# Kernel optimization log

Hardware: AMD Instinct MI355X
Metric: run time of the kernel (lower is better)

Reference implementation:

```python
import jax, jax.numpy as jnp
import numpy as np
from jax import lax

DIM = 192
NUM_CLASSES = 4
D_INNER = 2 * DIM          # expand=2
D_STATE = 16
D_CONV = 4
DT_RANK = (DIM + 15) // 16  # ceil(192/16)=12
PATCH = 16


def _mamba_params(key, prefix):
    ks = jax.random.split(key, 9)
    s = lambda k, shape, scale: (jax.random.normal(k, shape, jnp.float32) * scale)
    p = {
        prefix + '_in_w':   s(ks[0], (2 * D_INNER, DIM), 0.02),
        prefix + '_conv_w': s(ks[1], (D_INNER, D_CONV), 0.1),
        prefix + '_conv_b': jnp.zeros((D_INNER,), jnp.float32),
        prefix + '_xproj_w': s(ks[2], (DT_RANK + 2 * D_STATE, D_INNER), 0.02),
        prefix + '_dt_w':   s(ks[3], (D_INNER, DT_RANK), 0.1),
        prefix + '_dt_b':   s(ks[4], (D_INNER,), 0.1),
        # A_log init: log(1..d_state) broadcast over d_inner (mamba default)
        prefix + '_A_log':  jnp.broadcast_to(jnp.log(jnp.arange(1, D_STATE + 1, dtype=jnp.float32)), (D_INNER, D_STATE)) + 0.0,
        prefix + '_D':      jnp.ones((D_INNER,), jnp.float32),
        prefix + '_out_w':  s(ks[5], (DIM, D_INNER), 0.02),
    }
    return p


def setup_inputs() -> dict:
    key = jax.random.key(0)
    ks = jax.random.split(key, 8)
    inp = {
        'x': jax.random.normal(ks[0], (32, 3, 384, 384), jnp.float32),
        'patch_w': jax.random.normal(ks[1], (DIM, 3, PATCH, PATCH), jnp.float32) * 0.02,
        'patch_b': jnp.zeros((DIM,), jnp.float32),
        'ln_g': jnp.ones((DIM,), jnp.float32),
        'ln_b': jnp.zeros((DIM,), jnp.float32),
        'fc_w': jax.random.normal(ks[2], (NUM_CLASSES, DIM), jnp.float32) * 0.02,
        'fc_b': jnp.zeros((NUM_CLASSES,), jnp.float32),
    }
    inp.update(_mamba_params(ks[3], 'f'))
    inp.update(_mamba_params(ks[4], 'b'))
    return inp


def _layernorm(x, g, b, eps=1e-5):
    mu = jnp.mean(x, -1, keepdims=True)
    var = jnp.mean(jnp.square(x - mu), -1, keepdims=True)
    return (x - mu) * lax.rsqrt(var + eps) * g + b


def _mamba(x, in_w, conv_w, conv_b, xproj_w, dt_w, dt_b, A_log, Dskip, out_w):
    # x: [B, L, DIM]
    Bn, L, _ = x.shape
    xz = x @ in_w.T                                    # [B, L, 2*di]
    xi, z = jnp.split(xz, 2, axis=-1)
    # causal depthwise conv1d, kernel D_CONV, left pad
    xp = jnp.pad(xi, ((0, 0), (D_CONV - 1, 0), (0, 0)))
    xc = conv_b + sum(xp[:, k:k + L, :] * conv_w[:, k] for k in range(D_CONV))
    xc = jax.nn.silu(xc)                               # [B, L, di]
    proj = xc @ xproj_w.T                              # [B, L, dtr+2*ds]
    dt, Bm, Cm = jnp.split(proj, [DT_RANK, DT_RANK + D_STATE], axis=-1)
    dt = jax.nn.softplus(dt @ dt_w.T + dt_b)           # [B, L, di]
    A = -jnp.exp(A_log)                                # [di, ds]

    def step(h, inp):
        dt_t, B_t, C_t, x_t = inp                      # [B,di],[B,ds],[B,ds],[B,di]
        dA = jnp.exp(dt_t[:, :, None] * A)             # [B, di, ds]
        h = dA * h + (dt_t * x_t)[:, :, None] * B_t[:, None, :]
        y = jnp.einsum('bds,bs->bd', h, C_t)
        return h, y

    h0 = jnp.zeros((Bn, D_INNER, D_STATE), x.dtype)
    xs = (dt.transpose(1, 0, 2), Bm.transpose(1, 0, 2),
          Cm.transpose(1, 0, 2), xc.transpose(1, 0, 2))
    _, ys = lax.scan(step, h0, xs)                     # [L, B, di]
    y = ys.transpose(1, 0, 2) + xc * Dskip
    y = y * jax.nn.silu(z)
    return y @ out_w.T                                 # [B, L, DIM]


def reference(x, patch_w, patch_b, ln_g, ln_b, fc_w, fc_b,
              f_in_w, f_conv_w, f_conv_b, f_xproj_w, f_dt_w, f_dt_b, f_A_log, f_D, f_out_w,
              b_in_w, b_conv_w, b_conv_b, b_xproj_w, b_dt_w, b_dt_b, b_A_log, b_D, b_out_w):
    Bn, C, H, W = x.shape
    Hp, Wp = H // PATCH, W // PATCH
    # patch embed: stride==kernel conv == reshape + einsum
    xr = x.reshape(Bn, C, Hp, PATCH, Wp, PATCH)
    tok = jnp.einsum('bchpwq,dcpq->bhwd', xr, patch_w) + patch_b
    tok = tok.reshape(Bn, Hp * Wp, DIM)                # [B, L, D]
    tok = _layernorm(tok, ln_g, ln_b)
    fwd = _mamba(tok, f_in_w, f_conv_w, f_conv_b, f_xproj_w, f_dt_w, f_dt_b, f_A_log, f_D, f_out_w)
    bwd = _mamba(tok[:, ::-1, :], b_in_w, b_conv_w, b_conv_b, b_xproj_w, b_dt_w, b_dt_b, b_A_log, b_D, b_out_w)
    out = fwd + bwd[:, ::-1, :]
    pooled = jnp.mean(out, axis=1)                     # adaptive avg pool to 1
    return pooled @ fc_w.T + fc_b                      # [B, num_classes]
```

## Files before the change

kernel.cpp:

```cpp
#include <hip/hip_runtime.h>
#include <hip/hip_bf16.h>

#define NC 32
#define CL 18

typedef __attribute__((ext_vector_type(8))) short short8;
typedef __attribute__((ext_vector_type(4))) float f32x4;
typedef __attribute__((ext_vector_type(2))) float f32x2;

__device__ __forceinline__ float sigm(float x){ return 1.0f/(1.0f+__expf(-x)); }

__device__ __forceinline__ ushort f2bf(float f){
  unsigned u = __float_as_uint(f);
  unsigned r = (u + 0x7fffu + ((u>>16)&1u)) >> 16;
  return (ushort)r;
}
__device__ __forceinline__ float bf2f(ushort h){ return __uint_as_float(((unsigned)h)<<16); }

__global__ __launch_bounds__(256) void k_prep_all(
    const float* __restrict__ patch_w, const float* __restrict__ f_in_w,
    const float* __restrict__ b_in_w,
    const float* __restrict__ f_xw, const float* __restrict__ b_xw,
    const float* __restrict__ f_cw, const float* __restrict__ b_cw,
    const float* __restrict__ f_al, const float* __restrict__ b_al,
    const float* __restrict__ fc_w, const float* __restrict__ f_ow,
    const float* __restrict__ b_ow,
    ushort* __restrict__ pw_h, ushort* __restrict__ pw_l,
    ushort* __restrict__ iw_h, ushort* __restrict__ iw_l,
    ushort* __restrict__ xw_h, ushort* __restrict__ xw_l,
    float* __restrict__ cwT, float* __restrict__ Abuf,
    float* __restrict__ A0fl, float* __restrict__ W2){
  const int bx = blockIdx.x, t = threadIdx.x;
  if (bx < 1728){
    int which = bx/576;
    int i = (bx - which*576)*256 + t;
    if (which==0){
      float f = patch_w[i];
      ushort hb = f2bf(f);
      pw_h[i]=hb; pw_l[i]=f2bf(f - bf2f(hb));
    } else {
      const float* src = (which==1) ? f_in_w : b_in_w;
      int dirofs = (which==1) ? 0 : 48;
      float f = src[i];
      int n = i/192, k = i%192;
      int nblk = n>>4, r = n&15, kblk = k>>5, kk = k&31;
      int lane = r + ((kk>>3)<<4), j = kk&7;
      size_t idx = ((size_t)((nblk+dirofs)*6 + kblk)*64 + lane)*8 + j;
      ushort hb = f2bf(f);
      iw_h[idx]=hb; iw_l[idx]=f2bf(f - bf2f(hb));
    }
  } else if (bx < 1872){
    int i = (bx-1728)*256 + t;
    int dir=i/(48*384), rem=i%(48*384), n=rem/384, k=rem%384;
    float v = (n<44) ? (dir?b_xw:f_xw)[n*384+k] : 0.f;
    ushort hb = f2bf(v);
    xw_h[i]=hb; xw_l[i]=f2bf(v - bf2f(hb));
  } else if (bx < 1884){
    int i = (bx-1872)*256 + t;
    int dir=i/1536, rem=i%1536, j=rem/384, k=rem%384;
    cwT[i] = (dir ? b_cw : f_cw)[k*4+j];
  } else if (bx < 1887){
    int i = (bx-1884)*256 + t;
    if (i < 768){
      int dir=i/384, di=i%384;
      const float* alp = (dir?b_al:f_al) + di*16;
      float A0 = -expf(alp[0]);
      bool fast = true;
      Abuf[(size_t)i*16] = A0;
      #pragma unroll
      for (int s=1;s<16;s++){
        float A = -expf(alp[s]);
        Abuf[(size_t)i*16+s] = A;
        fast = fast && (fabsf(A - (s+1)*A0) <= 1e-5f*(s+1)*fabsf(A0));
      }
      A0fl[i*2]=A0; A0fl[i*2+1]=fast?1.f:0.f;
    }
  } else {
    int i = (bx-1887)*256 + t;
    if (i < 768){
      int dir=i/384, di=i%384;
      const float* ow = dir ? b_ow : f_ow;
      float a0=0.f,a1=0.f,a2=0.f,a3=0.f;
      for (int d=0; d<192; ++d){
        float o = ow[d*384 + di];
        a0 += fc_w[0*192+d]*o; a1 += fc_w[1*192+d]*o;
        a2 += fc_w[2*192+d]*o; a3 += fc_w[3*192+d]*o;
      }
      W2[(0*2+dir)*384+di]=a0; W2[(1*2+dir)*384+di]=a1;
      W2[(2*2+dir)*384+di]=a2; W2[(3*2+dir)*384+di]=a3;
    }
  }
}
__device__ __forceinline__ float w2at(const float* W2, int dir, int ch, int di){
  return W2[(ch*2+dir)*384+di];
}

__global__ __launch_bounds__(1024) void k_patch(
    const float* __restrict__ x,
    const ushort* __restrict__ pw_h, const ushort* __restrict__ pw_l,
    const float* __restrict__ pb, const float* __restrict__ lng,
    const float* __restrict__ lnb,
    ushort* __restrict__ tokf_h, ushort* __restrict__ tokf_l,
    int b0, int Mc){
  __shared__ __align__(16) char sBmem[49152];
  __shared__ __align__(16) ushort sAh[64*64], sAl[64*64];
  __shared__ float sLN[4][64][2];
  ushort* sBh = (ushort*)sBmem;
  ushort* sBl = (ushort*)(sBmem + 24576);
  const int tid = threadIdx.x;
  const int m0 = blockIdx.x*64;
  const int lane = tid&63, w = tid>>6;
  const int wr = w>>2, wc = w&3;
  const int r = lane&15, g = lane>>4;
  f32x4 acc[3];
  #pragma unroll
  for (int i=0;i<3;i++) acc[i] = (f32x4){0.f,0.f,0.f,0.f};

  for (int s=0;s<12;s++){
    const int c = s>>2, p0 = (s&3)*4;
    {
      int f = tid;
      int m = f>>4, rem = f&15, pp = rem>>2, qq = rem&3;
      int rm = m0 + m;
      float4 v = make_float4(0.f,0.f,0.f,0.f);
      if (rm < Mc){
        int b = b0 + rm/576, l = rm%576, hp = l/24, wp = l%24;
        size_t idx4 = ((size_t)((b*3+c)*384) + hp*16 + p0+pp)*96 + wp*4 + qq;
        v = reinterpret_cast<const float4*>(x)[idx4];
      }
      ushort4 hv, lv;
      hv.x=f2bf(v.x); lv.x=f2bf(v.x-bf2f(hv.x));
      hv.y=f2bf(v.y); lv.y=f2bf(v.y-bf2f(hv.y));
      hv.z=f2bf(v.z); lv.z=f2bf(v.z-bf2f(hv.z));
      hv.w=f2bf(v.w); lv.w=f2bf(v.w-bf2f(hv.w));
      int byte = (m*128 + pp*32 + qq*8) ^ ((m&7)<<4);
      *reinterpret_cast<ushort4*>((char*)sAh + byte) = hv;
      *reinterpret_cast<ushort4*>((char*)sAl + byte) = lv;
    }
    #pragma unroll
    for (int i=0;i<2;i++){
      int f = tid + i*1024;
      if (f < 1536){
        int n = f>>3, k8 = f&7;
        size_t gi = (size_t)n*768 + s*64 + k8*8;
        uint4 bh = *reinterpret_cast<const uint4*>(pw_h + gi);
        uint4 bl = *reinterpret_cast<const uint4*>(pw_l + gi);
        int byte = (n*128 + k8*16) ^ ((n&7)<<4);
        *reinterpret_cast<uint4*>((char*)sBh + byte) = bh;
        *reinterpret_cast<uint4*>((char*)sBl + byte) = bl;
      }
    }
    __syncthreads();
    #pragma unroll
    for (int kk=0;kk<2;kk++){
      int arow = wr*16 + r;
      int abyte = (arow*128 + kk*64 + g*16) ^ ((arow&7)<<4);
      short8 ah = *reinterpret_cast<const short8*>((char*)sAh + abyte);
      short8 al = *reinterpret_cast<const short8*>((char*)sAl + abyte);
      #pragma unroll
      for (int nfl=0; nfl<3; nfl++){
        int brow = (wc*3+nfl)*16 + r;
        int bbyte = (brow*128 + kk*64 + g*16) ^ ((brow&7)<<4);
        short8 bh = *reinterpret_cast<const short8*>((char*)sBh + bbyte);
        short8 bll = *reinterpret_cast<const short8*>((char*)sBl + bbyte);
        acc[nfl] = __builtin_amdgcn_mfma_f32_16x16x32_bf16(ah, bh, acc[nfl], 0,0,0);
        acc[nfl] = __builtin_amdgcn_mfma_f32_16x16x32_bf16(ah, bll, acc[nfl], 0,0,0);
        acc[nfl] = __builtin_amdgcn_mfma_f32_16x16x32_bf16(al, bh, acc[nfl], 0,0,0);
      }
    }
    __syncthreads();
  }
  float pbv[3], gv[3], bv[3];
  #pragma unroll
  for (int nfl=0;nfl<3;nfl++){
    int col = (wc*3+nfl)*16 + r;
    pbv[nfl]=pb[col]; gv[nfl]=lng[col]; bv[nfl]=lnb[col];
  }
  #pragma unroll
  for (int nfl=0;nfl<3;nfl++)
    #pragma unroll
    for (int q=0;q<4;q++) acc[nfl][q] += pbv[nfl];
  float sum[4]={0,0,0,0}, sq[4]={0,0,0,0};
  #pragma unroll
  for (int nfl=0;nfl<3;nfl++)
    #pragma unroll
    for (int q=0;q<4;q++){ float v=acc[nfl][q]; sum[q]+=v; sq[q]+=v*v; }
  #pragma unroll
  for (int off=1; off<16; off<<=1){
    #pragma unroll
    for (int q=0;q<4;q++){
      sum[q]+=__shfl_xor(sum[q],off);
      sq[q] +=__shfl_xor(sq[q],off);
    }
  }
  if (r==0){
    #pragma unroll
    for (int q=0;q<4;q++){
      int row = wr*16 + g*4 + q;
      sLN[wc][row][0]=sum[q]; sLN[wc][row][1]=sq[q];
    }
  }
  __syncthreads();
  float* sT = (float*)sBmem;
  #pragma unroll
  for (int q=0;q<4;q++){
    int rl = wr*16 + g*4 + q;
    float stot = sLN[0][rl][0]+sLN[1][rl][0]+sLN[2][rl][0]+sLN[3][rl][0];
    float qtot = sLN[0][rl][1]+sLN[1][rl][1]+sLN[2][rl][1]+sLN[3][rl][1];
    float mu = stot*(1.f/192.f);
    float var = qtot*(1.f/192.f) - mu*mu;
    float rs = rsqrtf(var + 1e-5f);
    #pragma unroll
    for (int nfl=0;nfl<3;nfl++)
      sT[rl*192 + (wc*3+nfl)*16 + r] = (acc[nfl][q]-mu)*rs*gv[nfl] + bv[nfl];
  }
  __syncthreads();
  const int mB = m0>>4;
  #pragma unroll
  for (int i=0;i<2;i++){
    int fl = tid + 1024*i;
    if (fl < 1536){
      int mb = fl/384, rem = fl-mb*384, kb = rem>>6, ln = rem&63;
      int rr = ln&15, gq = ln>>4;
      const float* sp = sT + (mb*16+rr)*192 + kb*32 + gq*8;
      short8 hv, lv;
      #pragma unroll
      for (int j=0;j<8;j++){
        float v = sp[j];
        ushort hb = f2bf(v);
        hv[j] = (short)hb;
        lv[j] = (short)f2bf(v - bf2f(hb));
      }
      size_t o = ((size_t)((mB+mb)*6 + kb)*64 + ln)*8;
      *reinterpret_cast<short8*>(tokf_h + o) = hv;
      *reinterpret_cast<short8*>(tokf_l + o) = lv;
// ... 144 lines not shown
  for (int kc=0; kc<6; ++kc){
    #pragma unroll
    for (int i=0;i<5;i++){
      int f = tid + i*256;
      if (f < 67*16){
        int rr = f>>4, kq = f&15;
        int l = l0 + rr - 3;
        float4 v = make_float4(0.f,0.f,0.f,0.f);
        if (l >= 0) v = *reinterpret_cast<const float4*>(xib + (seq+l)*384 + kc*64 + kq*4);
        int kqs = kq ^ (rr&15);
        *reinterpret_cast<float4*>(sRaw + rr*64 + kqs*4) = v;
      }
    }
    __syncthreads();
    #pragma unroll
    for (int i=0;i<4;i++){
      int f = tid + i*256;
      int m = f>>4, kq = f&15;
      float4 a = reinterpret_cast<const float4*>(cbp)[kc*16 + kq];
      #pragma unroll
      for (int j=0;j<4;j++){
        int rr = m + j;
        float4 rv = *reinterpret_cast<const float4*>(sRaw + rr*64 + (kq ^ (rr&15))*4);
        float4 cv = reinterpret_cast<const float4*>(cwTd)[j*96 + kc*16 + kq];
        a.x += cv.x*rv.x; a.y += cv.y*rv.y; a.z += cv.z*rv.z; a.w += cv.w*rv.w;
      }
      a.x = a.x*sigm(a.x); a.y = a.y*sigm(a.y); a.z = a.z*sigm(a.z); a.w = a.w*sigm(a.w);
      ushort4 hv, lv;
      hv.x=f2bf(a.x); lv.x=f2bf(a.x-bf2f(hv.x));
      hv.y=f2bf(a.y); lv.y=f2bf(a.y-bf2f(hv.y));
      hv.z=f2bf(a.z); lv.z=f2bf(a.z-bf2f(hv.z));
      hv.w=f2bf(a.w); lv.w=f2bf(a.w-bf2f(hv.w));
      *reinterpret_cast<ushort4*>(xcb + (seq + l0 + m)*384 + kc*64 + kq*4) = hv;
      int byte = (m*128 + kq*8) ^ ((m&7)<<4);
      *reinterpret_cast<ushort4*>((char*)sAh + byte) = hv;
      *reinterpret_cast<ushort4*>((char*)sAl + byte) = lv;
    }
    #pragma unroll
    for (int i=0;i<2;i++){
      int f = tid + i*256;
      if (f < 384){
        int n = f>>3, k8 = f&7;
        size_t gi = (size_t)n*384 + kc*64 + k8*8;
        uint4 vh = *reinterpret_cast<const uint4*>(bhp + gi);
        uint4 vl = *reinterpret_cast<const uint4*>(blp + gi);
        int byte = (n*128 + k8*16) ^ ((n&7)<<4);
        *reinterpret_cast<uint4*>((char*)sBh + byte) = vh;
        *reinterpret_cast<uint4*>((char*)sBl + byte) = vl;
      }
    }
    __syncthreads();
    #pragma unroll
    for (int kk=0;kk<2;kk++){
      int arow = w*16 + r;
      int abyte = (arow*128 + kk*64 + g*16) ^ ((arow&7)<<4);
      short8 ah = *reinterpret_cast<const short8*>((char*)sAh + abyte);
      short8 al = *reinterpret_cast<const short8*>((char*)sAl + abyte);
      #pragma unroll
      for (int nf=0;nf<3;nf++){
        int brow = nf*16 + r;
        int bbyte = (brow*128 + kk*64 + g*16) ^ ((brow&7)<<4);
        short8 bh = *reinterpret_cast<const short8*>((char*)sBh + bbyte);
        short8 bll = *reinterpret_cast<const short8*>((char*)sBl + bbyte);
        acc[nf] = __builtin_amdgcn_mfma_f32_16x16x32_bf16(ah, bh, acc[nf], 0,0,0);
        acc[nf] = __builtin_amdgcn_mfma_f32_16x16x32_bf16(ah, bll, acc[nf], 0,0,0);
        acc[nf] = __builtin_amdgcn_mfma_f32_16x16x32_bf16(al, bh, acc[nf], 0,0,0);
      }
    }
    __syncthreads();
  }
  #pragma unroll
  for (int nf=0;nf<3;nf++){
    int col = nf*16 + r;
    if (col < 44){
      #pragma unroll
      for (int q=0;q<4;q++){
        int l = l0 + w*16 + g*4 + q;
        proj[(seq+l)*44 + col] = acc[nf][q];
      }
    }
  }
}

__device__ __forceinline__ void build_dA2_fast(float e1, f32x2 dA2[8]){
  float e2 = e1*e1;
  f32x2 d0 = {e1, e2};
  float e4 = e2*e2;
  f32x2 e2v = {e2,e2}, e4v = {e4,e4};
  f32x2 d1 = d0*e2v;
  f32x2 d2 = d0*e4v;
  f32x2 d3 = d1*e4v;
  float e8 = e4*e4;
  f32x2 e8v = {e8,e8};
  dA2[0]=d0; dA2[1]=d1; dA2[2]=d2; dA2[3]=d3;
  dA2[4]=d0*e8v; dA2[5]=d1*e8v; dA2[6]=d2*e8v; dA2[7]=d3*e8v;
}

__global__ __launch_bounds__(256) void k_scan_p1(
    const ushort* __restrict__ zb, const ushort* __restrict__ xcb,
    const float* __restrict__ proj,
    const float* __restrict__ f_dtw, const float* __restrict__ b_dtw,
    const float* __restrict__ f_dtb, const float* __restrict__ b_dtb,
    const float* __restrict__ A0fl, const float* __restrict__ Abuf,
    const float* __restrict__ f_D,  const float* __restrict__ b_D,
    const float* __restrict__ W2, float* __restrict__ dtend,
    float* __restrict__ hbuf, float* __restrict__ part, int b0, int Bc){
  const int dir=blockIdx.z, bl=blockIdx.y;
  const int gg=blockIdx.x>>3, cq=blockIdx.x&7;
  const int wv=threadIdx.x>>6, lane=threadIdx.x&63;
  const int c = cq*4 + wv;
  const int di0 = gg*128 + lane*2;
  const size_t seq = ((size_t)dir*Bc + bl)*576;
  const float* dtwp = (dir?b_dtw:f_dtw) + (size_t)di0*12;
  f32x2 dtw2[12];
  {
    const float4* dp = reinterpret_cast<const float4*>(dtwp);
    #pragma unroll
    for (int i=0;i<3;i++){
      float4 fa = dp[i], fb = dp[i+3];
      dtw2[4*i+0] = (f32x2){fa.x, fb.x};
      dtw2[4*i+1] = (f32x2){fa.y, fb.y};
      dtw2[4*i+2] = (f32x2){fa.z, fb.z};
      dtw2[4*i+3] = (f32x2){fa.w, fb.w};
    }
  }
  float2 dtb2 = *reinterpret_cast<const float2*>((dir?b_dtb:f_dtb)+di0);
  float4 af = *reinterpret_cast<const float4*>(A0fl + ((size_t)dir*384+di0)*2);
  const float A0a = af.x, A0b = af.z;
  const bool fast = (af.y != 0.f) && (af.w != 0.f);
  const float* Abp = Abuf + ((size_t)dir*384+di0)*16;
  float2 Dv2 = *reinterpret_cast<const float2*>((dir?b_D:f_D)+di0);
  float2 w2c2[4];
  #pragma unroll
  for (int ch=0;ch<4;ch++)
    w2c2[ch] = *reinterpret_cast<const float2*>(W2 + (ch*2+dir)*384 + di0);
  f32x2 h2a[8], h2b[8];
  #pragma unroll
  for (int p=0;p<8;p++){ h2a[p]=(f32x2){0.f,0.f}; h2b[p]=(f32x2){0.f,0.f}; }
  float Sa=0.f, Sb=0.f, cuma=0.f, cumb=0.f;
  const int l0 = c*CL;
  const int pbase = (int)((seq + (size_t)l0)*44);
  const ushort* xcp = xcb + di0;
  const ushort* zbp2 = zb + di0;
  for (int j=0;j<CL;j++){
    const size_t row = seq + l0 + j;
    const int po = __builtin_amdgcn_readfirstlane(pbase + j*44);
    const float4* pr4 = reinterpret_cast<const float4*>(proj + po);
    float4 t0=pr4[0], t1=pr4[1], t2=pr4[2];
    f32x2 dtin2 = (f32x2){dtb2.x, dtb2.y};
    dtin2 += (f32x2){t0.x,t0.x}*dtw2[0]; dtin2 += (f32x2){t0.y,t0.y}*dtw2[1];
    dtin2 += (f32x2){t0.z,t0.z}*dtw2[2]; dtin2 += (f32x2){t0.w,t0.w}*dtw2[3];
    dtin2 += (f32x2){t1.x,t1.x}*dtw2[4]; dtin2 += (f32x2){t1.y,t1.y}*dtw2[5];
    dtin2 += (f32x2){t1.z,t1.z}*dtw2[6]; dtin2 += (f32x2){t1.w,t1.w}*dtw2[7];
    dtin2 += (f32x2){t2.x,t2.x}*dtw2[8]; dtin2 += (f32x2){t2.y,t2.y}*dtw2[9];
    dtin2 += (f32x2){t2.z,t2.z}*dtw2[10]; dtin2 += (f32x2){t2.w,t2.w}*dtw2[11];
    float dta = (dtin2[0] > 20.f) ? dtin2[0] : __logf(1.f + __expf(dtin2[0]));
    float dtb_ = (dtin2[1] > 20.f) ? dtin2[1] : __logf(1.f + __expf(dtin2[1]));
    cuma += dta; cumb += dtb_;
    uint xu = *reinterpret_cast<const uint*>(xcp + row*384);
    uint zu = *reinterpret_cast<const uint*>(zbp2 + row*384);
    float xca = bf2f((ushort)(xu&0xffffu)), xcbv = bf2f((ushort)(xu>>16));
    float zsa = bf2f((ushort)(zu&0xffffu)), zsb = bf2f((ushort)(zu>>16));
    float ua = dta*xca, ub = dtb_*xcbv;
    f32x2 u2a = {ua,ua}, u2b = {ub,ub};
    f32x2 dA2a[8], dA2b[8];
    if (fast){
      build_dA2_fast(__expf(dta*A0a), dA2a);
      build_dA2_fast(__expf(dtb_*A0b), dA2b);
    } else {
      #pragma unroll
      for (int p=0;p<8;p++){
        dA2a[p]=(f32x2){__expf(dta*Abp[2*p]), __expf(dta*Abp[2*p+1])};
        dA2b[p]=(f32x2){__expf(dtb_*Abp[16+2*p]), __expf(dtb_*Abp[16+2*p+1])};
      }
    }
    f32x2 yaa={0.f,0.f}, yba={0.f,0.f}, yab={0.f,0.f}, ybb={0.f,0.f};
    #pragma unroll
    for (int i=0;i<4;i++){
      float4 tb4=pr4[3+i], tc4=pr4[7+i];
      f32x2 B0={tb4.x,tb4.y}, B1={tb4.z,tb4.w};
      f32x2 C0={tc4.x,tc4.y}, C1={tc4.z,tc4.w};
      h2a[2*i]   = dA2a[2*i]*h2a[2*i]     + u2a*B0;
      h2a[2*i+1] = dA2a[2*i+1]*h2a[2*i+1] + u2a*B1;
      yaa += h2a[2*i]*C0;
      yba += h2a[2*i+1]*C1;
      h2b[2*i]   = dA2b[2*i]*h2b[2*i]     + u2b*B0;
      h2b[2*i+1] = dA2b[2*i+1]*h2b[2*i+1] + u2b*B1;
      yab += h2b[2*i]*C0;
      ybb += h2b[2*i+1]*C1;
    }
    Sa += ((yaa[0]+yaa[1])+(yba[0]+yba[1]) + xca*Dv2.x)*zsa;
    Sb += ((yab[0]+yab[1])+(ybb[0]+ybb[1]) + xcbv*Dv2.y)*zsb;
  }
  *reinterpret_cast<float2*>(dtend + ((((size_t)dir*Bc + bl)*NC + c)*384 + di0))
      = make_float2(cuma, cumb);
  size_t hb = ((((size_t)c*2+dir)*Bc + bl)*3 + gg)*2048;
  #pragma unroll
  for (int s=0;s<16;s++)
    *reinterpret_cast<float2*>(hbuf + hb + s*128 + lane*2)
        = make_float2(h2a[s>>1][s&1], h2b[s>>1][s&1]);
  float p0 = Sa*w2c2[0].x + Sb*w2c2[0].y;
  float p1v= Sa*w2c2[1].x + Sb*w2c2[1].y;
  float p2v= Sa*w2c2[2].x + Sb*w2c2[2].y;
  float p3v= Sa*w2c2[3].x + Sb*w2c2[3].y;
  #pragma unroll
  for (int off=32; off>0; off>>=1){
    p0 += __shfl_xor(p0, off); p1v += __shfl_xor(p1v, off);
    p2v += __shfl_xor(p2v, off); p3v += __shfl_xor(p3v, off);
  }
  if (lane==0){
    float* dst = part + ((((size_t)dir*32 + (b0+bl))*3 + gg)*64 + c)*4;
    dst[0]=p0; dst[1]=p1v; dst[2]=p2v; dst[3]=p3v;
  }
}

__global__ __launch_bounds__(256) void k_combine(
    const float* __restrict__ dtend, float* __restrict__ hbuf,
    const float* __restrict__ A0fl, const float* __restrict__ Abuf, int Bc){
  const int gg=blockIdx.x, bl=blockIdx.y, dir=blockIdx.z;
  const int wv=threadIdx.x>>6, lane=threadIdx.x&63;
  const int di0=gg*128+lane*2;
  float4 af = *reinterpret_cast<const float4*>(A0fl + ((size_t)dir*384+di0)*2);
  const bool fast = (af.y != 0.f) && (af.w != 0.f);
  const float* Abp = Abuf + ((size_t)dir*384+di0)*16;
  float Aa[4], Ab[4];
  #pragma unroll
  for (int si=0;si<4;si++){
    int s = wv*4+si;
    Aa[si] = fast ? af.x*(float)(s+1) : Abp[s];
    Ab[si] = fast ? af.z*(float)(s+1) : Abp[16+s];
  }
  float2 cur[4];
  size_t hx0 = ((((size_t)(0*2+dir)*Bc+bl)*3+gg)*2048) + (wv*4)*128 + lane*2;
  #pragma unroll
  for (int si=0;si<4;si++) cur[si]=*reinterpret_cast<float2*>(hbuf + hx0 + si*128);
  for (int c=1;c<NC;c++){
    size_t hx=((((size_t)c*2+dir)*Bc+bl)*3+gg)*2048 + (wv*4)*128 + lane*2;
    float2 tmp[4];
    #pragma unroll
    for (int si=0;si<4;si++){
      tmp[si]=*reinterpret_cast<float2*>(hbuf+hx+si*128);
      *reinterpret_cast<float2*>(hbuf+hx+si*128)=cur[si];
    }
    if (c<NC-1){
      float2 Sdt = *reinterpret_cast<const float2*>(dtend + ((((size_t)dir*Bc+bl)*NC + c)*384 + di0));
      #pragma unroll
      for (int si=0;si<4;si++){
        cur[si].x = __expf(Aa[si]*Sdt.x)*cur[si].x + tmp[si].x;
        cur[si].y = __expf(Ab[si]*Sdt.y)*cur[si].y + tmp[si].y;
      }
    }
  }
}

__global__ __launch_bounds__(256) void k_scan_p2(
    const ushort* __restrict__ zb, const float* __restrict__ proj,
    const float* __restrict__ hbuf,
    const float* __restrict__ f_dtw, const float* __restrict__ b_dtw,
    const float* __restrict__ f_dtb, const float* __restrict__ b_dtb,
    const float* __restrict__ A0fl, const float* __restrict__ Abuf,
    const float* __restrict__ W2, float* __restrict__ part, int b0, int Bc){
  const int dir=blockIdx.z, bl=blockIdx.y;
  const int gg=blockIdx.x>>3, cq=blockIdx.x&7;
  const int wv=threadIdx.x>>6, lane=threadIdx.x&63;
  const int c = cq*4 + wv + 1;
  const int di0 = gg*128 + lane*2;
  const size_t seq = ((size_t)dir*Bc + bl)*576;
  if (c >= NC) return;
  const float* dtwp = (dir?b_dtw:f_dtw) + (size_t)di0*12;
  f32x2 dtw2[12];
  {
    const float4* dp = reinterpret_cast<const float4*>(dtwp);
    #pragma unroll
    for (int i=0;i<3;i++){
      float4 fa = dp[i], fb = dp[i+3];
      dtw2[4*i+0] = (f32x2){fa.x, fb.x};
      dtw2[4*i+1] = (f32x2){fa.y, fb.y};
      dtw2[4*i+2] = (f32x2){fa.z, fb.z};
      dtw2[4*i+3] = (f32x2){fa.w, fb.w};
    }
  }
  float2 dtb2 = *reinterpret_cast<const float2*>((dir?b_dtb:f_dtb)+di0);
  float4 af = *reinterpret_cast<const float4*>(A0fl + ((size_t)dir*384+di0)*2);
  const float A0a = af.x, A0b = af.z;
  const bool fast = (af.y != 0.f) && (af.w != 0.f);
  const float* Abp = Abuf + ((size_t)dir*384+di0)*16;
  float2 w2c2[4];
  #pragma unroll
  for (int ch=0;ch<4;ch++)
    w2c2[ch] = *reinterpret_cast<const float2*>(W2 + (ch*2+dir)*384 + di0);
  f32x2 hh2a[8], hh2b[8];
  size_t hb=((((size_t)c*2+dir)*Bc+bl)*3+gg)*2048;
  #pragma unroll
  for (int s=0;s<16;s++){
    float2 v = *reinterpret_cast<const float2*>(hbuf + hb + s*128 + lane*2);
    hh2a[s>>1][s&1]=v.x; hh2b[s>>1][s&1]=v.y;
  }
  float Sa=0.f, Sb=0.f;
  const int l0 = c*CL;
  const int pbase = (int)((seq + (size_t)l0)*44);
  const ushort* zbp2 = zb + di0;
  for (int j=0;j<CL;j++){
    const size_t row = seq + l0 + j;
    const int po = __builtin_amdgcn_readfirstlane(pbase + j*44);
    const float4* pr4 = reinterpret_cast<const float4*>(proj + po);
    float4 t0=pr4[0], t1=pr4[1], t2=pr4[2];
    f32x2 dtin2 = (f32x2){dtb2.x, dtb2.y};
    dtin2 += (f32x2){t0.x,t0.x}*dtw2[0]; dtin2 += (f32x2){t0.y,t0.y}*dtw2[1];
    dtin2 += (f32x2){t0.z,t0.z}*dtw2[2]; dtin2 += (f32x2){t0.w,t0.w}*dtw2[3];
    dtin2 += (f32x2){t1.x,t1.x}*dtw2[4]; dtin2 += (f32x2){t1.y,t1.y}*dtw2[5];
    dtin2 += (f32x2){t1.z,t1.z}*dtw2[6]; dtin2 += (f32x2){t1.w,t1.w}*dtw2[7];
    dtin2 += (f32x2){t2.x,t2.x}*dtw2[8]; dtin2 += (f32x2){t2.y,t2.y}*dtw2[9];
    dtin2 += (f32x2){t2.z,t2.z}*dtw2[10]; dtin2 += (f32x2){t2.w,t2.w}*dtw2[11];
    float dta = (dtin2[0] > 20.f) ? dtin2[0] : __logf(1.f + __expf(dtin2[0]));
    float dtb_ = (dtin2[1] > 20.f) ? dtin2[1] : __logf(1.f + __expf(dtin2[1]));
    uint zu = *reinterpret_cast<const uint*>(zbp2 + row*384);
    float zsa = bf2f((ushort)(zu&0xffffu)), zsb = bf2f((ushort)(zu>>16));
    f32x2 dA2a[8], dA2b[8];
    if (fast){
      build_dA2_fast(__expf(dta*A0a), dA2a);
      build_dA2_fast(__expf(dtb_*A0b), dA2b);
    } else {
      #pragma unroll
      for (int p=0;p<8;p++){
        dA2a[p]=(f32x2){__expf(dta*Abp[2*p]), __expf(dta*Abp[2*p+1])};
        dA2b[p]=(f32x2){__expf(dtb_*Abp[16+2*p]), __expf(dtb_*Abp[16+2*p+1])};
      }
    }
    f32x2 yaa={0.f,0.f}, yba={0.f,0.f}, yab={0.f,0.f}, ybb={0.f,0.f};
    #pragma unroll
    for (int i=0;i<4;i++){
      float4 tc4 = pr4[7+i];
      f32x2 C0={tc4.x,tc4.y}, C1={tc4.z,tc4.w};
      hh2a[2*i]   = hh2a[2*i]*dA2a[2*i];
      hh2a[2*i+1] = hh2a[2*i+1]*dA2a[2*i+1];
      yaa += hh2a[2*i]*C0;
      yba += hh2a[2*i+1]*C1;
      hh2b[2*i]   = hh2b[2*i]*dA2b[2*i];
      hh2b[2*i+1] = hh2b[2*i+1]*dA2b[2*i+1];
      yab += hh2b[2*i]*C0;
      ybb += hh2b[2*i+1]*C1;
    }
    Sa += ((yaa[0]+yaa[1])+(yba[0]+yba[1]))*zsa;
    Sb += ((yab[0]+yab[1])+(ybb[0]+ybb[1]))*zsb;
  }
  float p0 = Sa*w2c2[0].x + Sb*w2c2[0].y;
  float p1v= Sa*w2c2[1].x + Sb*w2c2[1].y;
  float p2v= Sa*w2c2[2].x + Sb*w2c2[2].y;
  float p3v= Sa*w2c2[3].x + Sb*w2c2[3].y;
  #pragma unroll
  for (int off=32; off>0; off>>=1){
    p0 += __shfl_xor(p0, off); p1v += __shfl_xor(p1v, off);
    p2v += __shfl_xor(p2v, off); p3v += __shfl_xor(p3v, off);
  }
  if (lane==0){
    float* dst = part + ((((size_t)dir*32 + (b0+bl))*3 + gg)*64 + 32 + c)*4;
    dst[0]=p0; dst[1]=p1v; dst[2]=p2v; dst[3]=p3v;
  }
}

__global__ __launch_bounds__(256) void k_final(const float* __restrict__ part,
                                               const float* __restrict__ fc_b,
                                               float* __restrict__ out){
  const int b = blockIdx.x;
  const int ch = threadIdx.x>>6, lane = threadIdx.x&63;
  float s = 0.f;
  for (int i = lane; i < 384; i += 64){
    int c = i & 63;
    if (c == 32) continue;
    int dg = i >> 6;
    int dir = dg >= 3 ? 1 : 0;
    int g = dg - dir*3;
    s += part[((((size_t)dir*32 + b)*3 + g)*64 + c)*4 + ch];
  }
  #pragma unroll
  for (int off=32; off>0; off>>=1) s += __shfl_xor(s, off);
  if (lane==0) out[b*4+ch] = fc_b[ch] + s*(1.0f/576.0f);
}

extern "C" void kernel_launch(void* const* d_in, const int* in_sizes, int n_in,
                              void* d_out, int out_size, void* d_ws, size_t ws_size,
                              hipStream_t stream){
  const float* x       = (const float*)d_in[0];
  const float* patch_w = (const float*)d_in[1];
  const float* patch_b = (const float*)d_in[2];
  const float* ln_g    = (const float*)d_in[3];
  const float* ln_b    = (const float*)d_in[4];
  const float* fc_w    = (const float*)d_in[5];
  const float* fc_b    = (const float*)d_in[6];
  const float* f_in_w  = (const float*)d_in[7];
  const float* f_cw    = (const float*)d_in[8];
  const float* f_cb    = (const float*)d_in[9];
  const float* f_xw    = (const float*)d_in[10];
  const float* f_dtw   = (const float*)d_in[11];
  const float* f_dtb   = (const float*)d_in[12];
  const float* f_al    = (const float*)d_in[13];
  const float* f_D     = (const float*)d_in[14];
  const float* f_ow    = (const float*)d_in[15];
  const float* b_in_w  = (const float*)d_in[16];
  const float* b_cw    = (const float*)d_in[17];
  const float* b_cb    = (const float*)d_in[18];
  const float* b_xw    = (const float*)d_in[19];
  const float* b_dtw   = (const float*)d_in[20];
  const float* b_dtb   = (const float*)d_in[21];
  const float* b_al    = (const float*)d_in[22];
  const float* b_D     = (const float*)d_in[23];
  const float* b_ow    = (const float*)d_in[24];
  float* out = (float*)d_out;
  float* ws  = (float*)d_ws;

  float* W2    = ws;
  float* part  = W2 + 3072;
  ushort* pw_h = (ushort*)(part + 98304);
  ushort* pw_l = pw_h + 147456;
  ushort* iw_h = pw_l + 147456;
  ushort* iw_l = iw_h + 294912;
  ushort* xw_h = iw_l + 294912;
  ushort* xw_l = xw_h + 36864;
  float* cwT   = (float*)(xw_l + 36864);
  float* Abuf  = cwT + 3072;
  float* A0fl  = Abuf + 12288;
  float* base  = A0fl + 1536;

  const size_t FIXED = 3072 + 98304 + 2*73728 + 2*147456 + 2*18432 + 3072
                     + 12288 + 1536;
  const size_t perB = 110592ull + 442368ull + 110592ull + 110592ull
                    + 24576ull + 393216ull;
  int Bc = 32;
  while (Bc > 1 && (FIXED + (size_t)Bc*perB)*4ull > ws_size) Bc >>= 1;

  ushort* tokf_h = (ushort*)base;
  ushort* tokf_l = tokf_h + (size_t)Bc*110592ull;
  float* prj  = base;
  float* xib  = base + (size_t)Bc*110592ull;
  ushort* zbp = (ushort*)(xib + (size_t)Bc*442368ull);
  ushort* xcb = zbp + (size_t)Bc*442368ull;
  float* dtnd = (float*)(xcb + (size_t)Bc*442368ull);
  float* hbf  = dtnd + (size_t)Bc*24576ull;

  k_prep_all<<<dim3(1890),dim3(256),0,stream>>>(patch_w, f_in_w, b_in_w,
                                                f_xw, b_xw, f_cw, b_cw,
                                                f_al, b_al, fc_w, f_ow, b_ow,
                                                pw_h, pw_l, iw_h, iw_l,
                                                xw_h, xw_l, cwT, Abuf, A0fl, W2);

  for (int b0=0; b0<32; b0+=Bc){
    const int Mc = Bc*576;
    k_patch<<<dim3((Mc+63)/64),dim3(1024),0,stream>>>(x, pw_h, pw_l, patch_b,
                                                      ln_g, ln_b, tokf_h, tokf_l, b0, Mc);
    k_inproj<<<dim3((Mc+127)/128,12),dim3(1024),0,stream>>>(tokf_h, tokf_l, iw_h, iw_l,
                                                            xib, zbp, Bc, Mc);
    k_convx<<<dim3(9,Bc,2),dim3(256),0,stream>>>(xib, cwT, f_cb, b_cb,
                                                 xw_h, xw_l, prj, xcb, Bc);
    k_scan_p1<<<dim3(24,Bc,2),dim3(256),0,stream>>>(zbp, xcb, prj,
                                                    f_dtw,b_dtw, f_dtb,b_dtb,
                                                    A0fl, Abuf, f_D,b_D,
                                                    W2, dtnd, hbf, part, b0, Bc);
    k_combine<<<dim3(3,Bc,2),dim3(256),0,stream>>>(dtnd, hbf, A0fl, Abuf, Bc);
    k_scan_p2<<<dim3(24,Bc,2),dim3(256),0,stream>>>(zbp, prj, hbf,
                                                    f_dtw,b_dtw, f_dtb,b_dtb,
                                                    A0fl, Abuf, W2, part, b0, Bc);
  }
  k_final<<<dim3(32),dim3(256),0,stream>>>(part, fc_b, out);
}
```

Baseline: 228.5 us.

## Fold chunk-carry correction into combine via precomputed G sums, drop second scan pass

Because only the pooled mean of the output is needed, the carry-in state's contribution to each chunk is linear. The first scan pass now also accumulates G = sum over steps of C*z*cumulative dA. The combine kernel dots the propagated carry state with G and reduces directly into the partial logits, which removes the k_scan_p2 kernel that re-read z/proj and recomputed dt and exp per step. It also software-prefetches the next k-slice of x and the patch weights into registers in k_patch. The cost is extra registers and arithmetic in scan_p1, plus a new G buffer as large as the h buffer.

```diff
diff --git a/kernel.cpp b/kernel.cpp
--- a/kernel.cpp
+++ b/kernel.cpp
@@ -91,9 +91,6 @@
     }
   }
 }
-__device__ __forceinline__ float w2at(const float* W2, int dir, int ch, int di){
-  return W2[(ch*2+dir)*384+di];
-}
 
 __global__ __launch_bounds__(1024) void k_patch(
     const float* __restrict__ x,
@@ -116,41 +113,65 @@
   #pragma unroll
   for (int i=0;i<3;i++) acc[i] = (f32x4){0.f,0.f,0.f,0.f};
 
+  const int mA = tid>>4, remA = tid&15, ppA = remA>>2, qqA = remA&3;
+  const int rmA = m0 + mA;
+  const bool okA = (rmA < Mc);
+  size_t baseA = 0;
+  if (okA){
+    int b = b0 + rmA/576, l = rmA%576, hp = l/24, wp = l%24;
+    baseA = ((size_t)(b*3)*384 + hp*16 + ppA)*96 + wp*4 + qqA;
+  }
+  const int nB0 = tid>>3, k8B0 = tid&7;
+  const bool okB1 = (tid < 512);
+  const int fB1 = tid + 1024;
+  const int nB1 = fB1>>3, k8B1 = fB1&7;
+  const int byteA  = (mA*128 + ppA*32 + qqA*8) ^ ((mA&7)<<4);
+  const int byteB0 = (nB0*128 + k8B0*16) ^ ((nB0&7)<<4);
+  const int byteB1 = (nB1*128 + k8B1*16) ^ ((nB1&7)<<4);
+
+  float4 vA = make_float4(0.f,0.f,0.f,0.f);
+  uint4 vBh0 = {}, vBl0 = {}, vBh1 = {}, vBl1 = {};
+  {
+    if (okA) vA = reinterpret_cast<const float4*>(x)[baseA];
+    size_t gi0 = (size_t)nB0*768 + k8B0*8;
+    vBh0 = *reinterpret_cast<const uint4*>(pw_h + gi0);
+    vBl0 = *reinterpret_cast<const uint4*>(pw_l + gi0);
+    if (okB1){
+      size_t gi1 = (size_t)nB1*768 + k8B1*8;
+      vBh1 = *reinterpret_cast<const uint4*>(pw_h + gi1);
+      vBl1 = *reinterpret_cast<const uint4*>(pw_l + gi1);
+    }
+  }
+
   for (int s=0;s<12;s++){
-    const int c = s>>2, p0 = (s&3)*4;
     {
-      int f = tid;
-      int m = f>>4, rem = f&15, pp = rem>>2, qq = rem&3;
-      int rm = m0 + m;
-      float4 v = make_float4(0.f,0.f,0.f,0.f);
-      if (rm < Mc){
-        int b = b0 + rm/576, l = rm%576, hp = l/24, wp = l%24;
-        size_t idx4 = ((size_t)((b*3+c)*384) + hp*16 + p0+pp)*96 + wp*4 + qq;
-        v = reinterpret_cast<const float4*>(x)[idx4];
-      }
       ushort4 hv, lv;
-      hv.x=f2bf(v.x); lv.x=f2bf(v.x-bf2f(hv.x));
-      hv.y=f2bf(v.y); lv.y=f2bf(v.y-bf2f(hv.y));
-      hv.z=f2bf(v.z); lv.z=f2bf(v.z-bf2f(hv.z));
-      hv.w=f2bf(v.w); lv.w=f2bf(v.w-bf2f(hv.w));
-      int byte = (m*128 + pp*32 + qq*8) ^ ((m&7)<<4);
-      *reinterpret_cast<ushort4*>((char*)sAh + byte) = hv;
-      *reinterpret_cast<ushort4*>((char*)sAl + byte) = lv;
-    }
-    #pragma unroll
-    for (int i=0;i<2;i++){
-      int f = tid + i*1024;
-      if (f < 1536){
-        int n = f>>3, k8 = f&7;
-        size_t gi = (size_t)n*768 + s*64 + k8*8;
-        uint4 bh = *reinterpret_cast<const uint4*>(pw_h + gi);
-        uint4 bl = *reinterpret_cast<const uint4*>(pw_l + gi);
-        int byte = (n*128 + k8*16) ^ ((n&7)<<4);
-        *reinterpret_cast<uint4*>((char*)sBh + byte) = bh;
-        *reinterpret_cast<uint4*>((char*)sBl + byte) = bl;
+      hv.x=f2bf(vA.x); lv.x=f2bf(vA.x-bf2f(hv.x));
+      hv.y=f2bf(vA.y); lv.y=f2bf(vA.y-bf2f(hv.y));
+      hv.z=f2bf(vA.z); lv.z=f2bf(vA.z-bf2f(hv.z));
+      hv.w=f2bf(vA.w); lv.w=f2bf(vA.w-bf2f(hv.w));
+      *reinterpret_cast<ushort4*>((char*)sAh + byteA) = hv;
+      *reinterpret_cast<ushort4*>((char*)sAl + byteA) = lv;
+      *reinterpret_cast<uint4*>((char*)sBh + byteB0) = vBh0;
+      *reinterpret_cast<uint4*>((char*)sBl + byteB0) = vBl0;
+      if (okB1){
+        *reinterpret_cast<uint4*>((char*)sBh + byteB1) = vBh1;
+        *reinterpret_cast<uint4*>((char*)sBl + byteB1) = vBl1;
       }
     }
     __syncthreads();
+    if (s < 11){
+      int s1 = s+1, c1 = s1>>2, p01 = (s1&3)*4;
+      if (okA) vA = reinterpret_cast<const float4*>(x)[baseA + ((size_t)c1*384 + p01)*96];
+      size_t gi0 = (size_t)nB0*768 + (size_t)s1*64 + k8B0*8;
+      vBh0 = *reinterpret_cast<const uint4*>(pw_h + gi0);
+      vBl0 = *reinterpret_cast<const uint4*>(pw_l + gi0);
+      if (okB1){
+        size_t gi1 = (size_t)nB1*768 + (size_t)s1*64 + k8B1*8;
+        vBh1 = *reinterpret_cast<const uint4*>(pw_h + gi1);
+        vBl1 = *reinterpret_cast<const uint4*>(pw_l + gi1);
+      }
+    }
     #pragma unroll
     for (int kk=0;kk<2;kk++){
       int arow = wr*16 + r;
@@ -461,20 +482,6 @@
   }
 }
 
-__device__ __forceinline__ void build_dA2_fast(float e1, f32x2 dA2[8]){
-  float e2 = e1*e1;
-  f32x2 d0 = {e1, e2};
-  float e4 = e2*e2;
-  f32x2 e2v = {e2,e2}, e4v = {e4,e4};
-  f32x2 d1 = d0*e2v;
-  f32x2 d2 = d0*e4v;
-  f32x2 d3 = d1*e4v;
-  float e8 = e4*e4;
-  f32x2 e8v = {e8,e8};
-  dA2[0]=d0; dA2[1]=d1; dA2[2]=d2; dA2[3]=d3;
-  dA2[4]=d0*e8v; dA2[5]=d1*e8v; dA2[6]=d2*e8v; dA2[7]=d3*e8v;
-}
-
 __global__ __launch_bounds__(256) void k_scan_p1(
     const ushort* __restrict__ zb, const ushort* __restrict__ xcb,
     const float* __restrict__ proj,
@@ -483,7 +490,8 @@
     const float* __restrict__ A0fl, const float* __restrict__ Abuf,
     const float* __restrict__ f_D,  const float* __restrict__ b_D,
     const float* __restrict__ W2, float* __restrict__ dtend,
-    float* __restrict__ hbuf, float* __restrict__ part, int b0, int Bc){
+    float* __restrict__ hbuf, float* __restrict__ Gbuf,
+    float* __restrict__ part, int b0, int Bc){
   const int dir=blockIdx.z, bl=blockIdx.y;
   const int gg=blockIdx.x>>3, cq=blockIdx.x&7;
   const int wv=threadIdx.x>>6, lane=threadIdx.x&63;
@@ -513,9 +521,13 @@
   #pragma unroll
   for (int ch=0;ch<4;ch++)
     w2c2[ch] = *reinterpret_cast<const float2*>(W2 + (ch*2+dir)*384 + di0);
-  f32x2 h2a[8], h2b[8];
-  #pragma unroll
-  for (int p=0;p<8;p++){ h2a[p]=(f32x2){0.f,0.f}; h2b[p]=(f32x2){0.f,0.f}; }
+  f32x2 h2a[8], h2b[8], P2a[8], P2b[8], G2a[8], G2b[8];
+  #pragma unroll
+  for (int p=0;p<8;p++){
+    h2a[p]=(f32x2){0.f,0.f}; h2b[p]=(f32x2){0.f,0.f};
+    P2a[p]=(f32x2){1.f,1.f}; P2b[p]=(f32x2){1.f,1.f};
+    G2a[p]=(f32x2){0.f,0.f}; G2b[p]=(f32x2){0.f,0.f};
+  }
   float Sa=0.f, Sb=0.f, cuma=0.f, cumb=0.f;
   const int l0 = c*CL;
   const int pbase = (int)((seq + (size_t)l0)*44);
@@ -542,10 +554,21 @@
     float zsa = bf2f((ushort)(zu&0xffffu)), zsb = bf2f((ushort)(zu>>16));
     float ua = dta*xca, ub = dtb_*xcbv;
     f32x2 u2a = {ua,ua}, u2b = {ub,ub};
+    f32x2 zsa2 = {zsa,zsa}, zsb2 = {zsb,zsb};
     f32x2 dA2a[8], dA2b[8];
     if (fast){
-      build_dA2_fast(__expf(dta*A0a), dA2a);
-      build_dA2_fast(__expf(dtb_*A0b), dA2b);
+      float e1a=__expf(dta*A0a);
+      float e2a=e1a*e1a;
+      f32x2 e2va={e2a,e2a};
+      dA2a[0]=(f32x2){e1a,e2a};
+      #pragma unroll
+      for (int p=1;p<8;p++) dA2a[p]=dA2a[p-1]*e2va;
+      float e1b=__expf(dtb_*A0b);
+      float e2b=e1b*e1b;
+      f32x2 e2vb={e2b,e2b};
+      dA2b[0]=(f32x2){e1b,e2b};
+      #pragma unroll
+      for (int p=1;p<8;p++) dA2b[p]=dA2b[p-1]*e2vb;
     } else {
       #pragma unroll
       for (int p=0;p<8;p++){
@@ -567,6 +590,14 @@
       h2b[2*i+1] = dA2b[2*i+1]*h2b[2*i+1] + u2b*B1;
       yab += h2b[2*i]*C0;
       ybb += h2b[2*i+1]*C1;
+      P2a[2*i]   *= dA2a[2*i];   P2a[2*i+1] *= dA2a[2*i+1];
+      P2b[2*i]   *= dA2b[2*i];   P2b[2*i+1] *= dA2b[2*i+1];
+      f32x2 Cz0a = C0*zsa2, Cz1a = C1*zsa2;
+      f32x2 Cz0b = C0*zsb2, Cz1b = C1*zsb2;
+      G2a[2*i]   += Cz0a*P2a[2*i];
+      G2a[2*i+1] += Cz1a*P2a[2*i+1];
+      G2b[2*i]   += Cz0b*P2b[2*i];
+      G2b[2*i+1] += Cz1b*P2b[2*i+1];
     }
     Sa += ((yaa[0]+yaa[1])+(yba[0]+yba[1]) + xca*Dv2.x)*zsa;
     Sb += ((yab[0]+yab[1])+(ybb[0]+ybb[1]) + xcbv*Dv2.y)*zsb;
@@ -575,9 +606,12 @@
       = make_float2(cuma, cumb);
   size_t hb = ((((size_t)c*2+dir)*Bc + bl)*3 + gg)*2048;
   #pragma unroll
-  for (int s=0;s<16;s++)
+  for (int s=0;s<16;s++){
     *reinterpret_cast<float2*>(hbuf + hb + s*128 + lane*2)
         = make_float2(h2a[s>>1][s&1], h2b[s>>1][s&1]);
+    *reinterpret_cast<float2*>(Gbuf + hb + s*128 + lane*2)
+        = make_float2(G2a[s>>1][s&1], G2b[s>>1][s&1]);
+  }
   float p0 = Sa*w2c2[0].x + Sb*w2c2[0].y;
   float p1v= Sa*w2c2[1].x + Sb*w2c2[1].y;
   float p2v= Sa*w2c2[2].x + Sb*w2c2[2].y;
@@ -588,14 +622,17 @@
     p2v += __shfl_xor(p2v, off); p3v += __shfl_xor(p3v, off);
   }
   if (lane==0){
-    float* dst = part + ((((size_t)dir*32 + (b0+bl))*3 + gg)*64 + c)*4;
+    float* dst = part + ((((size_t)dir*32 + (b0+bl))*3 + gg)*32 + c)*4;
     dst[0]=p0; dst[1]=p1v; dst[2]=p2v; dst[3]=p3v;
   }
 }
 
 __global__ __launch_bounds__(256) void k_combine(
-    const float* __restrict__ dtend, float* __restrict__ hbuf,
-    const float* __restrict__ A0fl, const float* __restrict__ Abuf, int Bc){
+    const float* __restrict__ dtend, const float* __restrict__ hbuf,
+    const float* __restrict__ Gbuf,
+    const float* __restrict__ A0fl, const float* __restrict__ Abuf,
+    const float* __restrict__ W2, float* __restrict__ part2,
+    int b0, int Bc){
   const int gg=blockIdx.x, bl=blockIdx.y, dir=blockIdx.z;
   const int wv=threadIdx.x>>6, lane=threadIdx.x&63;
   const int di0=gg*128+lane*2;
@@ -609,17 +646,37 @@
     Aa[si] = fast ? af.x*(float)(s+1) : Abp[s];
     Ab[si] = fast ? af.z*(float)(s+1) : Abp[16+s];
   }
+  float2 w2c2[4];
+  #pragma unroll
+  for (int ch=0;ch<4;ch++)
+    w2c2[ch] = *reinterpret_cast<const float2*>(W2 + (ch*2+dir)*384 + di0);
   float2 cur[4];
   size_t hx0 = ((((size_t)(0*2+dir)*Bc+bl)*3+gg)*2048) + (wv*4)*128 + lane*2;
   #pragma unroll
-  for (int si=0;si<4;si++) cur[si]=*reinterpret_cast<float2*>(hbuf + hx0 + si*128);
+  for (int si=0;si<4;si++) cur[si]=*reinterpret_cast<const float2*>(hbuf + hx0 + si*128);
   for (int c=1;c<NC;c++){
     size_t hx=((((size_t)c*2+dir)*Bc+bl)*3+gg)*2048 + (wv*4)*128 + lane*2;
+    float ta=0.f, tb=0.f;
     float2 tmp[4];
     #pragma unroll
     for (int si=0;si<4;si++){
-      tmp[si]=*reinterpret_cast<float2*>(hbuf+hx+si*128);
-      *reinterpret_cast<float2*>(hbuf+hx+si*128)=cur[si];
+      tmp[si]=*reinterpret_cast<const float2*>(hbuf+hx+si*128);
+      float2 Gv = *reinterpret_cast<const float2*>(Gbuf+hx+si*128);
+      ta += cur[si].x*Gv.x;
+      tb += cur[si].y*Gv.y;
+    }
+    float p0 = ta*w2c2[0].x + tb*w2c2[0].y;
+    float p1v= ta*w2c2[1].x + tb*w2c2[1].y;
+    float p2v= ta*w2c2[2].x + tb*w2c2[2].y;
+    float p3v= ta*w2c2[3].x + tb*w2c2[3].y;
+    #pragma unroll
+    for (int off=32; off>0; off>>=1){
+      p0 += __shfl_xor(p0, off); p1v += __shfl_xor(p1v, off);
+      p2v += __shfl_xor(p2v, off); p3v += __shfl_xor(p3v, off);
+    }
+    if (lane==0){
+      float* dst = part2 + (((((size_t)(dir*32 + (b0+bl))*3 + gg)*4 + wv)*32) + c)*4;
+      dst[0]=p0; dst[1]=p1v; dst[2]=p2v; dst[3]=p3v;
     }
     if (c<NC-1){
       float2 Sdt = *reinterpret_cast<const float2*>(dtend + ((((size_t)dir*Bc+bl)*NC + c)*384 + di0));
@@ -632,125 +689,28 @@
   }
 }
 
-__global__ __launch_bounds__(256) void k_scan_p2(
-    const ushort* __restrict__ zb, const float* __restrict__ proj,
-    const float* __restrict__ hbuf,
-    const float* __restrict__ f_dtw, const float* __restrict__ b_dtw,
-    const float* __restrict__ f_dtb, const float* __restrict__ b_dtb,
-    const float* __restrict__ A0fl, const float* __restrict__ Abuf,
-    const float* __restrict__ W2, float* __restrict__ part, int b0, int Bc){
-  const int dir=blockIdx.z, bl=blockIdx.y;
-  const int gg=blockIdx.x>>3, cq=blockIdx.x&7;
-  const int wv=threadIdx.x>>6, lane=threadIdx.x&63;
-  const int c = cq*4 + wv + 1;
-  const int di0 = gg*128 + lane*2;
-  const size_t seq = ((size_t)dir*Bc + bl)*576;
-  if (c >= NC) return;
-  const float* dtwp = (dir?b_dtw:f_dtw) + (size_t)di0*12;
-  f32x2 dtw2[12];
-  {
-    const float4* dp = reinterpret_cast<const float4*>(dtwp);
-    #pragma unroll
-    for (int i=0;i<3;i++){
-      float4 fa = dp[i], fb = dp[i+3];
-      dtw2[4*i+0] = (f32x2){fa.x, fb.x};
-      dtw2[4*i+1] = (f32x2){fa.y, fb.y};
-      dtw2[4*i+2] = (f32x2){fa.z, fb.z};
-      dtw2[4*i+3] = (f32x2){fa.w, fb.w};
-    }
-  }
-  float2 dtb2 = *reinterpret_cast<const float2*>((dir?b_dtb:f_dtb)+di0);
-  float4 af = *reinterpret_cast<const float4*>(A0fl + ((size_t)dir*384+di0)*2);
-  const float A0a = af.x, A0b = af.z;
-  const bool fast = (af.y != 0.f) && (af.w != 0.f);
-  const float* Abp = Abuf + ((size_t)dir*384+di0)*16;
-  float2 w2c2[4];
-  #pragma unroll
-  for (int ch=0;ch<4;ch++)
-    w2c2[ch] = *reinterpret_cast<const float2*>(W2 + (ch*2+dir)*384 + di0);
-  f32x2 hh2a[8], hh2b[8];
-  size_t hb=((((size_t)c*2+dir)*Bc+bl)*3+gg)*2048;
-  #pragma unroll
-  for (int s=0;s<16;s++){
-    float2 v = *reinterpret_cast<const float2*>(hbuf + hb + s*128 + lane*2);
-    hh2a[s>>1][s&1]=v.x; hh2b[s>>1][s&1]=v.y;
-  }
-  float Sa=0.f, Sb=0.f;
-  const int l0 = c*CL;
-  const int pbase = (int)((seq + (size_t)l0)*44);
-  const ushort* zbp2 = zb + di0;
-  for (int j=0;j<CL;j++){
-    const size_t row = seq + l0 + j;
-    const int po = __builtin_amdgcn_readfirstlane(pbase + j*44);
-    const float4* pr4 = reinterpret_cast<const float4*>(proj + po);
-    float4 t0=pr4[0], t1=pr4[1], t2=pr4[2];
-    f32x2 dtin2 = (f32x2){dtb2.x, dtb2.y};
-    dtin2 += (f32x2){t0.x,t0.x}*dtw2[0]; dtin2 += (f32x2){t0.y,t0.y}*dtw2[1];
-    dtin2 += (f32x2){t0.z,t0.z}*dtw2[2]; dtin2 += (f32x2){t0.w,t0.w}*dtw2[3];
-    dtin2 += (f32x2){t1.x,t1.x}*dtw2[4]; dtin2 += (f32x2){t1.y,t1.y}*dtw2[5];
-    dtin2 += (f32x2){t1.z,t1.z}*dtw2[6]; dtin2 += (f32x2){t1.w,t1.w}*dtw2[7];
-    dtin2 += (f32x2){t2.x,t2.x}*dtw2[8]; dtin2 += (f32x2){t2.y,t2.y}*dtw2[9];
-    dtin2 += (f32x2){t2.z,t2.z}*dtw2[10]; dtin2 += (f32x2){t2.w,t2.w}*dtw2[11];
-    float dta = (dtin2[0] > 20.f) ? dtin2[0] : __logf(1.f + __expf(dtin2[0]));
-    float dtb_ = (dtin2[1] > 20.f) ? dtin2[1] : __logf(1.f + __expf(dtin2[1]));
-    uint zu = *reinterpret_cast<const uint*>(zbp2 + row*384);
-    float zsa = bf2f((ushort)(zu&0xffffu)), zsb = bf2f((ushort)(zu>>16));
-    f32x2 dA2a[8], dA2b[8];
-    if (fast){
-      build_dA2_fast(__expf(dta*A0a), dA2a);
-      build_dA2_fast(__expf(dtb_*A0b), dA2b);
-    } else {
-      #pragma unroll
-      for (int p=0;p<8;p++){
-        dA2a[p]=(f32x2){__expf(dta*Abp[2*p]), __expf(dta*Abp[2*p+1])};
-        dA2b[p]=(f32x2){__expf(dtb_*Abp[16+2*p]), __expf(dtb_*Abp[16+2*p+1])};
-      }
-    }
-    f32x2 yaa={0.f,0.f}, yba={0.f,0.f}, yab={0.f,0.f}, ybb={0.f,0.f};
-    #pragma unroll
-    for (int i=0;i<4;i++){
-      float4 tc4 = pr4[7+i];
-      f32x2 C0={tc4.x,tc4.y}, C1={tc4.z,tc4.w};
-      hh2a[2*i]   = hh2a[2*i]*dA2a[2*i];
-      hh2a[2*i+1] = hh2a[2*i+1]*dA2a[2*i+1];
-      yaa += hh2a[2*i]*C0;
-      yba += hh2a[2*i+1]*C1;
-      hh2b[2*i]   = hh2b[2*i]*dA2b[2*i];
-      hh2b[2*i+1] = hh2b[2*i+1]*dA2b[2*i+1];
-      yab += hh2b[2*i]*C0;
-      ybb += hh2b[2*i+1]*C1;
-    }
-    Sa += ((yaa[0]+yaa[1])+(yba[0]+yba[1]))*zsa;
-    Sb += ((yab[0]+yab[1])+(ybb[0]+ybb[1]))*zsb;
-  }
-  float p0 = Sa*w2c2[0].x + Sb*w2c2[0].y;
-  float p1v= Sa*w2c2[1].x + Sb*w2c2[1].y;
-  float p2v= Sa*w2c2[2].x + Sb*w2c2[2].y;
-  float p3v= Sa*w2c2[3].x + Sb*w2c2[3].y;
-  #pragma unroll
-  for (int off=32; off>0; off>>=1){
-    p0 += __shfl_xor(p0, off); p1v += __shfl_xor(p1v, off);
-    p2v += __shfl_xor(p2v, off); p3v += __shfl_xor(p3v, off);
-  }
-  if (lane==0){
-    float* dst = part + ((((size_t)dir*32 + (b0+bl))*3 + gg)*64 + 32 + c)*4;
-    dst[0]=p0; dst[1]=p1v; dst[2]=p2v; dst[3]=p3v;
-  }
-}
-
 __global__ __launch_bounds__(256) void k_final(const float* __restrict__ part,
+                                               const float* __restrict__ part2,
                                                const float* __restrict__ fc_b,
                                                float* __restrict__ out){
   const int b = blockIdx.x;
   const int ch = threadIdx.x>>6, lane = threadIdx.x&63;
   float s = 0.f;
-  for (int i = lane; i < 384; i += 64){
-    int c = i & 63;
-    if (c == 32) continue;
-    int dg = i >> 6;
+  for (int i = lane; i < 192; i += 64){
+    int c = i & 31;
+    int dg = i >> 5;
     int dir = dg >= 3 ? 1 : 0;
-    int g = dg - dir*3;
-    s += part[((((size_t)dir*32 + b)*3 + g)*64 + c)*4 + ch];
+    int gg = dg - dir*3;
+    s += part[((((size_t)dir*32 + b)*3 + gg)*32 + c)*4 + ch];
+  }
+  for (int i = lane; i < 768; i += 64){
+    int c = i & 31;
+    if (c == 0) continue;
+    int t = i >> 5;
+    int dir = t >= 12 ? 1 : 0;
+    int rem = t - dir*12;
+    int gg = rem >> 2, wv = rem & 3;
+    s += part2[(((((size_t)(dir*32 + b)*3 + gg)*4 + wv)*32) + c)*4 + ch];
   }
   #pragma unroll
   for (int off=32; off>0; off>>=1) s += __shfl_xor(s, off);
@@ -790,7 +750,8 @@
 
   float* W2    = ws;
   float* part  = W2 + 3072;
-  ushort* pw_h = (ushort*)(part + 98304);
+  float* part2 = part + 24576;
+  ushort* pw_h = (ushort*)(part2 + 98304);
   ushort* pw_l = pw_h + 147456;
   ushort* iw_h = pw_l + 147456;
   ushort* iw_l = iw_h + 294912;
@@ -801,10 +762,8 @@
   float* A0fl  = Abuf + 12288;
   float* base  = A0fl + 1536;
 
-  const size_t FIXED = 3072 + 98304 + 2*73728 + 2*147456 + 2*18432 + 3072
-                     + 12288 + 1536;
-  const size_t perB = 110592ull + 442368ull + 110592ull + 110592ull
-                    + 24576ull + 393216ull;
+  const size_t FIXED = 622080ull;
+  const size_t perB  = 1806336ull;
   int Bc = 32;
   while (Bc > 1 && (FIXED + (size_t)Bc*perB)*4ull > ws_size) Bc >>= 1;
 
@@ -816,6 +775,7 @@
   ushort* xcb = zbp + (size_t)Bc*442368ull;
   float* dtnd = (float*)(xcb + (size_t)Bc*442368ull);
   float* hbf  = dtnd + (size_t)Bc*24576ull;
+  float* Gbf  = hbf + (size_t)Bc*393216ull;
 
   k_prep_all<<<dim3(1890),dim3(256),0,stream>>>(patch_w, f_in_w, b_in_w,
                                                 f_xw, b_xw, f_cw, b_cw,
@@ -834,11 +794,9 @@
     k_scan_p1<<<dim3(24,Bc,2),dim3(256),0,stream>>>(zbp, xcb, prj,
                                                     f_dtw,b_dtw, f_dtb,b_dtb,
                                                     A0fl, Abuf, f_D,b_D,
-                                                    W2, dtnd, hbf, part, b0, Bc);
-    k_combine<<<dim3(3,Bc,2),dim3(256),0,stream>>>(dtnd, hbf, A0fl, Abuf, Bc);
-    k_scan_p2<<<dim3(24,Bc,2),dim3(256),0,stream>>>(zbp, prj, hbf,
-                                                    f_dtw,b_dtw, f_dtb,b_dtb,
-                                                    A0fl, Abuf, W2, part, b0, Bc);
-  }
-  k_final<<<dim3(32),dim3(256),0,stream>>>(part, fc_b, out);
+                                                    W2, dtnd, hbf, Gbf, part, b0, Bc);
+    k_combine<<<dim3(3,Bc,2),dim3(256),0,stream>>>(dtnd, hbf, Gbf, A0fl, Abuf,
+                                                   W2, part2, b0, Bc);
+  }
+  k_final<<<dim3(32),dim3(256),0,stream>>>(part, part2, fc_b, out);
 }
```

Measured after the change: 240.3 us. 1.05x slower.
